# Performance work log

Measured on AMD Instinct MI355X. Metric: run time of the kernel, lower is better.

## Reference

```python
import jax, jax.numpy as jnp
import numpy as np

RES = 256
DEC = 8
NUM_MEAS = RES * RES // DEC  # 8192
BATCH = 4


def _bilinear_gather(img, coords):
    """grid_sample-style bilinear interpolation (align_corners=True, zero padding).
    img: [B, C, H, W]; coords: [M, 2] with (x, y) in pixel-centered units [-res/2, res/2].
    Returns [B, C, M]."""
    B, C, H, W = img.shape
    # normalize to [-1, 1] then map to pixel index space (align_corners=True)
    gx = (coords[:, 0] / (W / 2) + 1.0) * 0.5 * (W - 1)
    gy = (coords[:, 1] / (H / 2) + 1.0) * 0.5 * (H - 1)
    x0 = jnp.floor(gx)
    y0 = jnp.floor(gy)
    wx1 = gx - x0
    wx0 = 1.0 - wx1
    wy1 = gy - y0
    wy0 = 1.0 - wy1
    x0i = x0.astype(jnp.int32)
    y0i = y0.astype(jnp.int32)

    def tap(xi, yi, w):
        valid = ((xi >= 0) & (xi < W) & (yi >= 0) & (yi < H)).astype(img.dtype)
        xc = jnp.clip(xi, 0, W - 1)
        yc = jnp.clip(yi, 0, H - 1)
        v = img[:, :, yc, xc]  # [B, C, M] advanced-index gather
        return v * (w * valid)[None, None, :]

    return (tap(x0i, y0i, wx0 * wy0) + tap(x0i + 1, y0i, wx1 * wy0)
            + tap(x0i, y0i + 1, wx0 * wy1) + tap(x0i + 1, y0i + 1, wx1 * wy1))


def _nufft_adjoint(s, coords, N):
    """Exact adjoint non-uniform DFT (the math the gridding NUFFT approximates).
    s: [B, M] complex samples at k-space locations coords [M, 2] (pixel units, centered).
    out[b, y, x] = sum_m s[b,m] * exp(2j*pi*(kx_m*(x-N/2) + ky_m*(y-N/2))/N)."""
    n = jnp.arange(N, dtype=jnp.float32) - N / 2  # centered image coords
    two_pi = jnp.float32(2.0 * np.pi)
    Ex = jnp.exp(1j * (two_pi * coords[:, 0:1] * n[None, :] / N)).astype(jnp.complex64)  # [M, N]
    Ey = jnp.exp(1j * (two_pi * coords[:, 1:2] * n[None, :] / N)).astype(jnp.complex64)  # [M, N]
    t = s[:, :, None] * Ey[None, :, :]          # [B, M, H]
    return jnp.einsum('bmy,mx->byx', t, Ex)     # [B, H, W] complex64


def setup_inputs() -> dict:
    key = jax.random.key(0)
    k1, k2 = jax.random.split(key)
    inp = jax.random.normal(k1, (BATCH, 1, RES, RES, 2), dtype=jnp.float32)
    # gaussian trajectory init: randn * res / 6 (learnable parameter)
    x = jax.random.normal(k2, (NUM_MEAS, 2), dtype=jnp.float32) * (RES / 6.0)
    return {"input": inp, "x": x}


def reference(input, x):
    # [B,1,H,W,2] -> [B,2,H,W] (real/imag as channels)
    img = jnp.transpose(input, (0, 1, 4, 2, 3))[:, 0]
    B, C, H, W = img.shape
    sub_ksp = _bilinear_gather(img, x)                      # [B, 2, M]
    s = (sub_ksp[:, 0] + 1j * sub_ksp[:, 1]).astype(jnp.complex64)  # [B, M]
    out_c = _nufft_adjoint(s, x, H)                          # [B, H, W]
    out = jnp.stack([out_c.real, out_c.imag], axis=-1)       # [B, H, W, 2]
    return out[:, None]                                      # [B, 1, H, W, 2]
```

## Files before the change

### kernel.cpp

```cpp
#include <hip/hip_runtime.h>
#include <hip/hip_bf16.h>
#include <stdint.h>
#include <math.h>

#define RES     256
#define M_MEAS  8192
#define BATCH   4
#define KDIM    8192
#define ROWS    2048
#define NCOLS   288
#define SINOFF  144
#define SPLIT   16
#define KCHUNK  512
#define BM      128
#define BN      96
#define BK      64
#define NT      (KCHUNK / BK)

typedef __attribute__((ext_vector_type(8))) __bf16 bf16x8;
typedef __attribute__((ext_vector_type(8))) unsigned short u16x8;
typedef __attribute__((ext_vector_type(4))) float f32x4;
typedef __attribute__((ext_vector_type(2))) float f32x2;

#define OFF_A  262144
#define OFF_B  33816576
#define OFF_C  38535168

__device__ __forceinline__ unsigned short f2bf(float f) {
    unsigned u = __float_as_uint(f);
    u += 0x7FFFu + ((u >> 16) & 1u);
    return (unsigned short)(u >> 16);
}

__device__ __forceinline__ void lds_load16(const void* g, void* l) {
    __builtin_amdgcn_global_load_lds(
        (const __attribute__((address_space(1))) uint32_t*)(uintptr_t)g,
        (__attribute__((address_space(3))) uint32_t*)(uint32_t)(uintptr_t)l,
        16, 0, 0);
}

__global__ __launch_bounds__(256) void k_gather(const float* __restrict__ in,
                                                const float* __restrict__ xs,
                                                float* __restrict__ sRe,
                                                float* __restrict__ sIm) {
    int t = blockIdx.x * 256 + threadIdx.x;
    int b = t >> 13, m = t & (M_MEAS - 1);
    float kx = xs[2 * m + 0], ky = xs[2 * m + 1];
    float gx = (kx * (1.0f / 128.0f) + 1.0f) * 0.5f * 255.0f;
    float gy = (ky * (1.0f / 128.0f) + 1.0f) * 0.5f * 255.0f;
    float fx0 = floorf(gx), fy0 = floorf(gy);
    float wx1 = gx - fx0, wx0 = 1.0f - wx1;
    float wy1 = gy - fy0, wy0 = 1.0f - wy1;
    int x0 = (int)fx0, y0 = (int)fy0;
    float re = 0.0f, im = 0.0f;
#pragma unroll
    for (int dy = 0; dy < 2; ++dy) {
#pragma unroll
        for (int dx = 0; dx < 2; ++dx) {
            int xi = x0 + dx, yi = y0 + dy;
            bool v = (xi >= 0) && (xi < RES) && (yi >= 0) && (yi < RES);
            int xc = min(max(xi, 0), RES - 1);
            int yc = min(max(yi, 0), RES - 1);
            float w = (dx ? wx1 : wx0) * (dy ? wy1 : wy0) * (v ? 1.0f : 0.0f);
            const float* p = in + ((((size_t)b * RES + yc) * RES + xc) * 2);
            re += p[0] * w;
            im += p[1] * w;
        }
    }
    sRe[b * M_MEAS + m] = re;
    sIm[b * M_MEAS + m] = im;
}

__global__ __launch_bounds__(256) void k_buildAB(const float* __restrict__ xs,
                                                 const float* __restrict__ sRe,
                                                 const float* __restrict__ sIm,
                                                 unsigned short* __restrict__ A,
                                                 unsigned short* __restrict__ Bt) {
    int blk = blockIdx.x;
    if (blk < 1024) {
        int t = blk * 256 + threadIdx.x;
        int y  = t >> 10;
        int m0 = (t & 1023) * 8;
        float n = (float)(y - 128);
        float c[8], s_[8];
#pragma unroll
        for (int j = 0; j < 8; ++j) {
            float ky = xs[2 * (m0 + j) + 1];
            float u = ky * n * (1.0f / 256.0f);
            u -= rintf(u);
            float th = u * 6.28318530717958647692f;
            s_[j] = __sinf(th);
            c[j]  = __cosf(th);
        }
#pragma unroll
        for (int b = 0; b < BATCH; ++b) {
            u16x8 vr, vi;
#pragma unroll
            for (int j = 0; j < 8; ++j) {
                float sr = sRe[b * M_MEAS + m0 + j];
                float si = sIm[b * M_MEAS + m0 + j];
                vr[j] = f2bf(sr * c[j] - si * s_[j]);
                vi[j] = f2bf(sr * s_[j] + si * c[j]);
            }
            *(u16x8*)(A + ((size_t)b * 512 + y) * KDIM + m0)       = vr;
            *(u16x8*)(A + ((size_t)b * 512 + 256 + y) * KDIM + m0) = vi;
        }
    } else {
        int t = (blk - 1024) * 256 + threadIdx.x;
        int cidx = t >> 10;
        int m0 = (t & 1023) * 8;
        bool isCos = cidx < SINOFF;
        int u = isCos ? cidx : (cidx - SINOFF);
        u16x8 v;
        if (u > 128) {
            v = (u16x8){0, 0, 0, 0, 0, 0, 0, 0};
        } else {
            float nn = (float)u;
#pragma unroll
            for (int j = 0; j < 8; ++j) {
                float kx = xs[2 * (m0 + j) + 0];
                float ur = kx * nn * (1.0f / 256.0f);
                ur -= rintf(ur);
                float th = ur * 6.28318530717958647692f;
                v[j] = f2bf(isCos ? __cosf(th) : __sinf(th));
            }
        }
        *(u16x8*)(Bt + (size_t)cidx * KDIM + m0) = v;
    }
}

__global__ __launch_bounds__(256, 2) void k_gemm(const unsigned short* __restrict__ A,
                                                 const unsigned short* __restrict__ Bt,
                                                 float* __restrict__ Cp) {
    __shared__ __align__(16) unsigned short As[2][BM * BK];
    __shared__ __align__(16) unsigned short Bs[2][BN * BK];

    int bid   = blockIdx.x;
    int tile  = bid >> 4;
    int split = bid & 15;
    int tr = tile / 3, tc = tile - tr * 3;
    int row0 = tr * BM, col0 = tc * BN;
    int kbase = split * KCHUNK;
    int tid = threadIdx.x;
    int w = tid >> 6, l = tid & 63;
    int wr = w >> 1, wc = w & 1;

    f32x4 acc[4][3] = {};
    int lr = l & 15, lu = l >> 4;

#define STAGE(buf, k0)                                                            \
    do {                                                                          \
        _Pragma("unroll")                                                         \
        for (int q = 0; q < 4; ++q) {                                             \
            int U = q * 256 + tid;                                                \
            int r = U >> 3, u = U & 7;                                            \
            lds_load16(A + (size_t)(row0 + r) * KDIM + (k0) + ((u ^ (r & 7)) * 8),\
                       &As[buf][(size_t)U * 8]);                                  \
        }                                                                         \
        _Pragma("unroll")                                                         \
        for (int q = 0; q < 3; ++q) {                                             \
            int U = q * 256 + tid;                                                \
            int r = U >> 3, u = U & 7;                                            \
            lds_load16(Bt + (size_t)(col0 + r) * KDIM + (k0) + ((u ^ (r & 7)) * 8),\
                       &Bs[buf][(size_t)U * 8]);                                  \
        }                                                                         \
    } while (0)

    STAGE(0, kbase);
    STAGE(1, kbase + BK);

#pragma unroll
    for (int t = 0; t < NT; ++t) {
        int cur = t & 1;
        if (t < NT - 1) asm volatile("s_waitcnt vmcnt(7)" ::: "memory");
        else            asm volatile("s_waitcnt vmcnt(0)" ::: "memory");
        __builtin_amdgcn_sched_barrier(0);
        __builtin_amdgcn_s_barrier();
        __builtin_amdgcn_sched_barrier(0);

        bf16x8 af[2][4], bfr[2][3];
#pragma unroll
        for (int ks = 0; ks < 2; ++ks) {
#pragma unroll
            for (int i = 0; i < 4; ++i) {
                int row = wr * 64 + i * 16 + lr;
                af[ks][i] = *(const bf16x8*)(&As[cur][row * 64 + (((ks << 2) | lu) ^ (row & 7)) * 8]);
            }
#pragma unroll
            for (int j = 0; j < 3; ++j) {
                int row = wc * 48 + j * 16 + lr;
                bfr[ks][j] = *(const bf16x8*)(&Bs[cur][row * 64 + (((ks << 2) | lu) ^ (row & 7)) * 8]);
            }
        }
        __builtin_amdgcn_sched_barrier(0);
        asm volatile("s_waitcnt lgkmcnt(0)" ::: "memory");
        __builtin_amdgcn_sched_barrier(0);
        __builtin_amdgcn_s_barrier();
        __builtin_amdgcn_sched_barrier(0);

        if (t < NT - 2) STAGE(cur, kbase + (t + 2) * BK);

#pragma unroll
        for (int ks = 0; ks < 2; ++ks)
#pragma unroll
            for (int i = 0; i < 4; ++i)
#pragma unroll
                for (int j = 0; j < 3; ++j)
                    acc[i][j] = __builtin_amdgcn_mfma_f32_16x16x32_bf16(af[ks][i], bfr[ks][j], acc[i][j], 0, 0, 0);
    }
#undef STAGE

    float* Cb = Cp + (size_t)split * ROWS * NCOLS;
#pragma unroll
    for (int i = 0; i < 4; ++i) {
#pragma unroll
        for (int j = 0; j < 3; ++j) {
            int colg = col0 + wc * 48 + j * 16 + (l & 15);
#pragma unroll
            for (int v = 0; v < 4; ++v) {
                int rowg = row0 + wr * 64 + i * 16 + (l >> 4) * 4 + v;
                Cb[(size_t)rowg * NCOLS + colg] = acc[i][j][v];
            }
        }
    }
}

__global__ __launch_bounds__(256) void k_combine(const float* __restrict__ Cp,
                                                 float* __restrict__ out) {
    int t = blockIdx.x * 256 + threadIdx.x;
    int x = t & 255, y = (t >> 8) & 255, b = t >> 16;
    int n = x - 128;
    int u = (n < 0) ? -n : n;
    float sg = (n < 0) ? -1.0f : 1.0f;
    size_t rRe = ((size_t)b * 512 + y) * NCOLS;
    size_t rIm = rRe + (size_t)256 * NCOLS;
    float cr = 0.0f, sr = 0.0f, ci = 0.0f, si = 0.0f;
#pragma unroll
    for (int s2 = 0; s2 < SPLIT; ++s2) {
        const float* Cb = Cp + (size_t)s2 * ROWS * NCOLS;
        cr += Cb[rRe + u];
        sr += Cb[rRe + SINOFF + u];
        ci += Cb[rIm + u];
        si += Cb[rIm + SINOFF + u];
    }
    float re = cr - sg * si;
    float im = sg * sr + ci;
    ((f32x2*)out)[t] = (f32x2){re, im};
}

extern "C" void kernel_launch(void* const* d_in, const int* in_sizes, int n_in,
                              void* d_out, int out_size, void* d_ws, size_t ws_size,
                              hipStream_t stream) {
    const float* in = (const float*)d_in[0];
    const float* xs = (const float*)d_in[1];
    float* out = (float*)d_out;
    char* ws = (char*)d_ws;

    float* sRe = (float*)ws;
    float* sIm = sRe + BATCH * M_MEAS;
    unsigned short* A  = (unsigned short*)(ws + OFF_A);
    unsigned short* Bt = (unsigned short*)(ws + OFF_B);
    float* Cp = (float*)(ws + OFF_C);

    k_gather <<<128,         256, 0, stream>>>(in, xs, sRe, sIm);
    k_buildAB<<<1024 + 1152, 256, 0, stream>>>(xs, sRe, sIm, A, Bt);
    k_gemm   <<<768,         256, 0, stream>>>(A, Bt, Cp);
    k_combine<<<1024,        256, 0, stream>>>(Cp, out);
}
```

Baseline: 48.59 us.

## Generate A operand on the fly inside GEMM and fuse gather with B build

The GEMM no longer reads a precomputed 32 MB bf16 A matrix. Each block stages the ky, sRe and sIm values for its K chunk into LDS and builds the phase-rotated A tile directly in LDS, using sin/cos recurrences over rows. The gather and B-table kernels are merged into one launch, the tile shape changes to 128x144, and the split-K partials are stored as bf16 to halve combine traffic. The costs are extra ALU/transcendental work in the GEMM loop, accumulated error from the recurrence, and bf16 rounding of the partial sums before the reduction.

Result: faster. 41.15 us (-15.3%).

```diff
diff --git a/kernel.cpp b/kernel.cpp
--- a/kernel.cpp
+++ b/kernel.cpp
@@ -5,31 +5,38 @@
 
 #define RES     256
 #define M_MEAS  8192
-#define BATCH   4
 #define KDIM    8192
-#define ROWS    2048
+#define ROWSC   2048
 #define NCOLS   288
 #define SINOFF  144
 #define SPLIT   16
 #define KCHUNK  512
 #define BM      128
-#define BN      96
+#define BN      144
 #define BK      64
 #define NT      (KCHUNK / BK)
+#define TWO_PI  6.28318530717958647692f
 
 typedef __attribute__((ext_vector_type(8))) __bf16 bf16x8;
 typedef __attribute__((ext_vector_type(8))) unsigned short u16x8;
 typedef __attribute__((ext_vector_type(4))) float f32x4;
 typedef __attribute__((ext_vector_type(2))) float f32x2;
 
-#define OFF_A  262144
-#define OFF_B  33816576
-#define OFF_C  38535168
+#define OFF_SRE 0
+#define OFF_SIM 131072
+#define OFF_KY  262144
+#define OFF_B   294912
+#define OFF_C   5013504
 
 __device__ __forceinline__ unsigned short f2bf(float f) {
     unsigned u = __float_as_uint(f);
     u += 0x7FFFu + ((u >> 16) & 1u);
     return (unsigned short)(u >> 16);
+}
+
+__device__ __forceinline__ float bf2f(unsigned short v) {
+    unsigned u = ((unsigned)v) << 16;
+    return __uint_as_float(u);
 }
 
 __device__ __forceinline__ void lds_load16(const void* g, void* l) {
@@ -39,74 +46,43 @@
         16, 0, 0);
 }
 
-__global__ __launch_bounds__(256) void k_gather(const float* __restrict__ in,
-                                                const float* __restrict__ xs,
-                                                float* __restrict__ sRe,
-                                                float* __restrict__ sIm) {
-    int t = blockIdx.x * 256 + threadIdx.x;
-    int b = t >> 13, m = t & (M_MEAS - 1);
-    float kx = xs[2 * m + 0], ky = xs[2 * m + 1];
-    float gx = (kx * (1.0f / 128.0f) + 1.0f) * 0.5f * 255.0f;
-    float gy = (ky * (1.0f / 128.0f) + 1.0f) * 0.5f * 255.0f;
-    float fx0 = floorf(gx), fy0 = floorf(gy);
-    float wx1 = gx - fx0, wx0 = 1.0f - wx1;
-    float wy1 = gy - fy0, wy0 = 1.0f - wy1;
-    int x0 = (int)fx0, y0 = (int)fy0;
-    float re = 0.0f, im = 0.0f;
-#pragma unroll
-    for (int dy = 0; dy < 2; ++dy) {
-#pragma unroll
-        for (int dx = 0; dx < 2; ++dx) {
-            int xi = x0 + dx, yi = y0 + dy;
-            bool v = (xi >= 0) && (xi < RES) && (yi >= 0) && (yi < RES);
-            int xc = min(max(xi, 0), RES - 1);
-            int yc = min(max(yi, 0), RES - 1);
-            float w = (dx ? wx1 : wx0) * (dy ? wy1 : wy0) * (v ? 1.0f : 0.0f);
-            const float* p = in + ((((size_t)b * RES + yc) * RES + xc) * 2);
-            re += p[0] * w;
-            im += p[1] * w;
-        }
-    }
-    sRe[b * M_MEAS + m] = re;
-    sIm[b * M_MEAS + m] = im;
-}
-
-__global__ __launch_bounds__(256) void k_buildAB(const float* __restrict__ xs,
-                                                 const float* __restrict__ sRe,
-                                                 const float* __restrict__ sIm,
-                                                 unsigned short* __restrict__ A,
-                                                 unsigned short* __restrict__ Bt) {
+__global__ __launch_bounds__(256) void k_prep(const float* __restrict__ in,
+                                              const float* __restrict__ xs,
+                                              float* __restrict__ sRe,
+                                              float* __restrict__ sIm,
+                                              float* __restrict__ kyc,
+                                              unsigned short* __restrict__ Bt) {
     int blk = blockIdx.x;
-    if (blk < 1024) {
+    if (blk < 128) {
         int t = blk * 256 + threadIdx.x;
-        int y  = t >> 10;
-        int m0 = (t & 1023) * 8;
-        float n = (float)(y - 128);
-        float c[8], s_[8];
-#pragma unroll
-        for (int j = 0; j < 8; ++j) {
-            float ky = xs[2 * (m0 + j) + 1];
-            float u = ky * n * (1.0f / 256.0f);
-            u -= rintf(u);
-            float th = u * 6.28318530717958647692f;
-            s_[j] = __sinf(th);
-            c[j]  = __cosf(th);
-        }
-#pragma unroll
-        for (int b = 0; b < BATCH; ++b) {
-            u16x8 vr, vi;
-#pragma unroll
-            for (int j = 0; j < 8; ++j) {
-                float sr = sRe[b * M_MEAS + m0 + j];
-                float si = sIm[b * M_MEAS + m0 + j];
-                vr[j] = f2bf(sr * c[j] - si * s_[j]);
-                vi[j] = f2bf(sr * s_[j] + si * c[j]);
-            }
-            *(u16x8*)(A + ((size_t)b * 512 + y) * KDIM + m0)       = vr;
-            *(u16x8*)(A + ((size_t)b * 512 + 256 + y) * KDIM + m0) = vi;
-        }
+        int b = t >> 13, m = t & (M_MEAS - 1);
+        float kx = xs[2 * m + 0], ky = xs[2 * m + 1];
+        if (t < M_MEAS) kyc[t] = xs[2 * t + 1];
+        float gx = (kx * (1.0f / 128.0f) + 1.0f) * 0.5f * 255.0f;
+        float gy = (ky * (1.0f / 128.0f) + 1.0f) * 0.5f * 255.0f;
+        float fx0 = floorf(gx), fy0 = floorf(gy);
+        float wx1 = gx - fx0, wx0 = 1.0f - wx1;
+        float wy1 = gy - fy0, wy0 = 1.0f - wy1;
+        int x0 = (int)fx0, y0 = (int)fy0;
+        float re = 0.0f, im = 0.0f;
+#pragma unroll
+        for (int dy = 0; dy < 2; ++dy) {
+#pragma unroll
+            for (int dx = 0; dx < 2; ++dx) {
+                int xi = x0 + dx, yi = y0 + dy;
+                bool v = (xi >= 0) && (xi < RES) && (yi >= 0) && (yi < RES);
+                int xc = min(max(xi, 0), RES - 1);
+                int yc = min(max(yi, 0), RES - 1);
+                float w = (dx ? wx1 : wx0) * (dy ? wy1 : wy0) * (v ? 1.0f : 0.0f);
+                const float* p = in + ((((size_t)b * RES + yc) * RES + xc) * 2);
+                re += p[0] * w;
+                im += p[1] * w;
+            }
+        }
+        sRe[b * M_MEAS + m] = re;
+        sIm[b * M_MEAS + m] = im;
     } else {
-        int t = (blk - 1024) * 256 + threadIdx.x;
+        int t = (blk - 128) * 256 + threadIdx.x;
         int cidx = t >> 10;
         int m0 = (t & 1023) * 8;
         bool isCos = cidx < SINOFF;
@@ -121,7 +97,7 @@
                 float kx = xs[2 * (m0 + j) + 0];
                 float ur = kx * nn * (1.0f / 256.0f);
                 ur -= rintf(ur);
-                float th = ur * 6.28318530717958647692f;
+                float th = ur * TWO_PI;
                 v[j] = f2bf(isCos ? __cosf(th) : __sinf(th));
             }
         }
@@ -129,103 +105,147 @@
     }
 }
 
-__global__ __launch_bounds__(256, 2) void k_gemm(const unsigned short* __restrict__ A,
+__global__ __launch_bounds__(256, 2) void k_gemm(const float* __restrict__ sReG,
+                                                 const float* __restrict__ sImG,
+                                                 const float* __restrict__ kyG,
                                                  const unsigned short* __restrict__ Bt,
-                                                 float* __restrict__ Cp) {
+                                                 unsigned short* __restrict__ Cp) {
     __shared__ __align__(16) unsigned short As[2][BM * BK];
     __shared__ __align__(16) unsigned short Bs[2][BN * BK];
-
-    int bid   = blockIdx.x;
-    int tile  = bid >> 4;
-    int split = bid & 15;
-    int tr = tile / 3, tc = tile - tr * 3;
-    int row0 = tr * BM, col0 = tc * BN;
+    __shared__ __align__(16) float sbuf[3 * KCHUNK];
+
+    int bid = blockIdx.x;
+    int tc = bid & 1, rest = bid >> 1;
+    int tr = rest & 15, split = rest >> 4;
+    int col0 = tc * BN;
     int kbase = split * KCHUNK;
+    int yhalf = tr & 1, isIm = (tr >> 1) & 1, batch = tr >> 2;
     int tid = threadIdx.x;
     int w = tid >> 6, l = tid & 63;
-    int wr = w >> 1, wc = w & 1;
-
-    f32x4 acc[4][3] = {};
     int lr = l & 15, lu = l >> 4;
 
-#define STAGE(buf, k0)                                                            \
+    f32x4 acc[2][9] = {};
+
+#define STAGE_B(buf, kt)                                                          \
     do {                                                                          \
         _Pragma("unroll")                                                         \
-        for (int q = 0; q < 4; ++q) {                                             \
-            int U = q * 256 + tid;                                                \
+        for (int q = 0; q < 5; ++q) {                                             \
+            int U = q * 256 + tid; if (U >= 1152) U -= 1152;                      \
             int r = U >> 3, u = U & 7;                                            \
-            lds_load16(A + (size_t)(row0 + r) * KDIM + (k0) + ((u ^ (r & 7)) * 8),\
-                       &As[buf][(size_t)U * 8]);                                  \
-        }                                                                         \
-        _Pragma("unroll")                                                         \
-        for (int q = 0; q < 3; ++q) {                                             \
-            int U = q * 256 + tid;                                                \
-            int r = U >> 3, u = U & 7;                                            \
-            lds_load16(Bt + (size_t)(col0 + r) * KDIM + (k0) + ((u ^ (r & 7)) * 8),\
-                       &Bs[buf][(size_t)U * 8]);                                  \
+            lds_load16(Bt + (size_t)(col0 + r) * KDIM + kbase + (kt) * BK         \
+                          + ((u ^ (r & 7)) * 8),                                  \
+                       &Bs[buf][U * 8]);                                          \
         }                                                                         \
     } while (0)
 
-    STAGE(0, kbase);
-    STAGE(1, kbase + BK);
-
-#pragma unroll
+#define GEN_A(buf, kt)                                                            \
+    do {                                                                          \
+        int p = tid & 31, g = tid >> 5;                                           \
+        int mi = (kt) * BK + p * 2;                                               \
+        float2 kyp = *(const float2*)&sbuf[mi];                                   \
+        float2 srp = *(const float2*)&sbuf[KCHUNK + mi];                          \
+        float2 sip = *(const float2*)&sbuf[2 * KCHUNK + mi];                      \
+        float n0 = (float)(yhalf * 128 + g * 16 - 128);                           \
+        float c0, s0, c1, s1, cs0, ss0, cs1, ss1;                                 \
+        { float u = kyp.x * n0 * (1.0f/256.0f); u -= rintf(u);                    \
+          s0 = __sinf(u * TWO_PI); c0 = __cosf(u * TWO_PI); }                     \
+        { float u = kyp.x * (1.0f/256.0f); u -= rintf(u);                         \
+          ss0 = __sinf(u * TWO_PI); cs0 = __cosf(u * TWO_PI); }                   \
+        { float u = kyp.y * n0 * (1.0f/256.0f); u -= rintf(u);                    \
+          s1 = __sinf(u * TWO_PI); c1 = __cosf(u * TWO_PI); }                     \
+        { float u = kyp.y * (1.0f/256.0f); u -= rintf(u);                         \
+          ss1 = __sinf(u * TWO_PI); cs1 = __cosf(u * TWO_PI); }                   \
+        _Pragma("unroll")                                                         \
+        for (int j = 0; j < 16; ++j) {                                            \
+            int r = g * 16 + j;                                                   \
+            float v0 = isIm ? fmaf(srp.x, s0, sip.x * c0)                         \
+                            : fmaf(srp.x, c0, -(sip.x * s0));                     \
+            float v1 = isIm ? fmaf(srp.y, s1, sip.y * c1)                         \
+                            : fmaf(srp.y, c1, -(sip.y * s1));                     \
+            unsigned pk = (unsigned)f2bf(v0) | ((unsigned)f2bf(v1) << 16);        \
+            *(unsigned*)&As[buf][r * 64 + (((p >> 2) ^ (r & 7)) * 8) + (p & 3) * 2] = pk; \
+            float nc0 = fmaf(c0, cs0, -(s0 * ss0));                               \
+            float ns0 = fmaf(s0, cs0,  (c0 * ss0));                               \
+            c0 = nc0; s0 = ns0;                                                   \
+            float nc1 = fmaf(c1, cs1, -(s1 * ss1));                               \
+            float ns1 = fmaf(s1, cs1,  (c1 * ss1));                               \
+            c1 = nc1; s1 = ns1;                                                   \
+        }                                                                         \
+    } while (0)
+
+#pragma unroll
+    for (int q = 0; q < 2; ++q) {
+        int V = q * 256 + tid; if (V >= 384) V -= 384;
+        int rg = V >> 7, idx = V & 127;
+        const float* s = (rg == 0) ? kyG
+                       : (rg == 1) ? (sReG + (size_t)batch * M_MEAS)
+                                   : (sImG + (size_t)batch * M_MEAS);
+        lds_load16(s + kbase + idx * 4, &sbuf[V * 4]);
+    }
+    STAGE_B(0, 0);
+    asm volatile("s_waitcnt vmcnt(5)" ::: "memory");
+    __builtin_amdgcn_s_barrier();
+    GEN_A(0, 0);
+    asm volatile("s_waitcnt vmcnt(0) lgkmcnt(0)" ::: "memory");
+    __builtin_amdgcn_sched_barrier(0);
+    __builtin_amdgcn_s_barrier();
+
     for (int t = 0; t < NT; ++t) {
         int cur = t & 1;
-        if (t < NT - 1) asm volatile("s_waitcnt vmcnt(7)" ::: "memory");
-        else            asm volatile("s_waitcnt vmcnt(0)" ::: "memory");
+        if (t < NT - 1) {
+            STAGE_B(cur ^ 1, t + 1);
+            GEN_A(cur ^ 1, t + 1);
+        }
+
+        bf16x8 af[2][2], bfr[2][9];
+#pragma unroll
+        for (int ks = 0; ks < 2; ++ks) {
+            int uu = ks * 4 + lu;
+#pragma unroll
+            for (int i = 0; i < 2; ++i) {
+                int r = w * 32 + i * 16 + lr;
+                af[ks][i] = *(const bf16x8*)&As[cur][r * 64 + ((uu ^ (r & 7)) * 8)];
+            }
+#pragma unroll
+            for (int j = 0; j < 9; ++j) {
+                int r = j * 16 + lr;
+                bfr[ks][j] = *(const bf16x8*)&Bs[cur][r * 64 + ((uu ^ (r & 7)) * 8)];
+            }
+        }
+        asm volatile("s_waitcnt lgkmcnt(0)" ::: "memory");
+        __builtin_amdgcn_sched_barrier(0);
+        __builtin_amdgcn_s_setprio(1);
+#pragma unroll
+        for (int ks = 0; ks < 2; ++ks)
+#pragma unroll
+            for (int i = 0; i < 2; ++i)
+#pragma unroll
+                for (int j = 0; j < 9; ++j)
+                    acc[i][j] = __builtin_amdgcn_mfma_f32_16x16x32_bf16(af[ks][i], bfr[ks][j], acc[i][j], 0, 0, 0);
+        __builtin_amdgcn_s_setprio(0);
+        asm volatile("s_waitcnt vmcnt(0)" ::: "memory");
         __builtin_amdgcn_sched_barrier(0);
         __builtin_amdgcn_s_barrier();
-        __builtin_amdgcn_sched_barrier(0);
-
-        bf16x8 af[2][4], bfr[2][3];
-#pragma unroll
-        for (int ks = 0; ks < 2; ++ks) {
-#pragma unroll
-            for (int i = 0; i < 4; ++i) {
-                int row = wr * 64 + i * 16 + lr;
-                af[ks][i] = *(const bf16x8*)(&As[cur][row * 64 + (((ks << 2) | lu) ^ (row & 7)) * 8]);
-            }
-#pragma unroll
-            for (int j = 0; j < 3; ++j) {
-                int row = wc * 48 + j * 16 + lr;
-                bfr[ks][j] = *(const bf16x8*)(&Bs[cur][row * 64 + (((ks << 2) | lu) ^ (row & 7)) * 8]);
-            }
-        }
-        __builtin_amdgcn_sched_barrier(0);
-        asm volatile("s_waitcnt lgkmcnt(0)" ::: "memory");
-        __builtin_amdgcn_sched_barrier(0);
-        __builtin_amdgcn_s_barrier();
-        __builtin_amdgcn_sched_barrier(0);
-
-        if (t < NT - 2) STAGE(cur, kbase + (t + 2) * BK);
-
-#pragma unroll
-        for (int ks = 0; ks < 2; ++ks)
-#pragma unroll
-            for (int i = 0; i < 4; ++i)
-#pragma unroll
-                for (int j = 0; j < 3; ++j)
-                    acc[i][j] = __builtin_amdgcn_mfma_f32_16x16x32_bf16(af[ks][i], bfr[ks][j], acc[i][j], 0, 0, 0);
-    }
-#undef STAGE
-
-    float* Cb = Cp + (size_t)split * ROWS * NCOLS;
-#pragma unroll
-    for (int i = 0; i < 4; ++i) {
-#pragma unroll
-        for (int j = 0; j < 3; ++j) {
-            int colg = col0 + wc * 48 + j * 16 + (l & 15);
+    }
+#undef STAGE_B
+#undef GEN_A
+
+    unsigned short* Cb = Cp + (size_t)split * ROWSC * NCOLS;
+#pragma unroll
+    for (int i = 0; i < 2; ++i) {
+#pragma unroll
+        for (int j = 0; j < 9; ++j) {
+            int colg = col0 + j * 16 + lr;
 #pragma unroll
             for (int v = 0; v < 4; ++v) {
-                int rowg = row0 + wr * 64 + i * 16 + (l >> 4) * 4 + v;
-                Cb[(size_t)rowg * NCOLS + colg] = acc[i][j][v];
-            }
-        }
-    }
-}
-
-__global__ __launch_bounds__(256) void k_combine(const float* __restrict__ Cp,
+                int rowg = tr * BM + w * 32 + i * 16 + lu * 4 + v;
+                Cb[(size_t)rowg * NCOLS + colg] = f2bf(acc[i][j][v]);
+            }
+        }
+    }
+}
+
+__global__ __launch_bounds__(256) void k_combine(const unsigned short* __restrict__ Cp,
                                                  float* __restrict__ out) {
     int t = blockIdx.x * 256 + threadIdx.x;
     int x = t & 255, y = (t >> 8) & 255, b = t >> 16;
@@ -237,11 +257,11 @@
     float cr = 0.0f, sr = 0.0f, ci = 0.0f, si = 0.0f;
 #pragma unroll
     for (int s2 = 0; s2 < SPLIT; ++s2) {
-        const float* Cb = Cp + (size_t)s2 * ROWS * NCOLS;
-        cr += Cb[rRe + u];
-        sr += Cb[rRe + SINOFF + u];
-        ci += Cb[rIm + u];
-        si += Cb[rIm + SINOFF + u];
+        const unsigned short* Cb = Cp + (size_t)s2 * ROWSC * NCOLS;
+        cr += bf2f(Cb[rRe + u]);
+        sr += bf2f(Cb[rRe + SINOFF + u]);
+        ci += bf2f(Cb[rIm + u]);
+        si += bf2f(Cb[rIm + SINOFF + u]);
     }
     float re = cr - sg * si;
     float im = sg * sr + ci;
@@ -256,14 +276,13 @@
     float* out = (float*)d_out;
     char* ws = (char*)d_ws;
 
-    float* sRe = (float*)ws;
-    float* sIm = sRe + BATCH * M_MEAS;
-    unsigned short* A  = (unsigned short*)(ws + OFF_A);
+    float* sRe = (float*)(ws + OFF_SRE);
+    float* sIm = (float*)(ws + OFF_SIM);
+    float* kyc = (float*)(ws + OFF_KY);
     unsigned short* Bt = (unsigned short*)(ws + OFF_B);
-    float* Cp = (float*)(ws + OFF_C);
-
-    k_gather <<<128,         256, 0, stream>>>(in, xs, sRe, sIm);
-    k_buildAB<<<1024 + 1152, 256, 0, stream>>>(xs, sRe, sIm, A, Bt);
-    k_gemm   <<<768,         256, 0, stream>>>(A, Bt, Cp);
-    k_combine<<<1024,        256, 0, stream>>>(Cp, out);
-}
+    unsigned short* Cp = (unsigned short*)(ws + OFF_C);
+
+    k_prep   <<<128 + 1152, 256, 0, stream>>>(in, xs, sRe, sIm, kyc, Bt);
+    k_gemm   <<<512,        256, 0, stream>>>(sRe, sIm, kyc, Bt, Cp);
+    k_combine<<<1024,       256, 0, stream>>>(Cp, out);
+}
```
